# Optimization experiments

Measured on AMD Instinct MI355X. Metric: run time of the kernel, lower is better.

The kernel has to match this reference:

```python
import jax, jax.numpy as jnp
import numpy as np

B = 8192
DIMS = [1024, 1024, 1024, 1024]  # input, hidden0, hidden1, output
RANK = 64


def _apg_layer(x, Wm, bm, U, V, b, activate):
    # hyper-net (MLP_Layer with no hidden units == single Linear): generates rank*rank weights per sample
    w = (x @ Wm.T + bm).reshape(x.shape[0], RANK, RANK)   # [B, r, r]
    u = x @ U.T                                           # U_matrix: [B, r]
    # (u.unsqueeze(-1) * w).sum(-2) == per-sample matvec
    h = jnp.einsum('br,brs->bs', u, w)                    # [B, r]
    out = h @ V.T + b                                     # V_matrix + static bias: [B, out]
    return jax.nn.relu(out) if activate else out


def setup_inputs() -> dict:
    key = jax.random.key(0)
    ks = jax.random.split(key, 16)
    inp = {"x": jax.random.normal(ks[0], (B, DIMS[0]), dtype=jnp.float32)}
    ki = 1
    for l in range(3):
        din, dout = DIMS[l], DIMS[l + 1]
        inp[f"Wm{l}"] = jax.random.normal(ks[ki], (RANK * RANK, din), dtype=jnp.float32) * (1.0 / np.sqrt(din)); ki += 1
        inp[f"bm{l}"] = jnp.zeros((RANK * RANK,), dtype=jnp.float32)
        inp[f"U{l}"] = jax.random.normal(ks[ki], (RANK, din), dtype=jnp.float32) * (1.0 / np.sqrt(din)); ki += 1
        inp[f"V{l}"] = jax.random.normal(ks[ki], (dout, RANK), dtype=jnp.float32) * (1.0 / np.sqrt(RANK)); ki += 1
        inp[f"b{l}"] = jnp.zeros((dout,), dtype=jnp.float32)
    return inp


def reference(x, Wm0, bm0, U0, V0, b0, Wm1, bm1, U1, V1, b1, Wm2, bm2, U2, V2, b2):
    h = _apg_layer(x, Wm0, bm0, U0, V0, b0, activate=True)   # hidden layer 0 + ReLU
    h = _apg_layer(h, Wm1, bm1, U1, V1, b1, activate=True)   # hidden layer 1 + ReLU
    out = _apg_layer(h, Wm2, bm2, U2, V2, b2, activate=False)  # output layer, no activation
    return out
```

## Files before the change

kernel.cpp:

```cpp
#include <hip/hip_runtime.h>
#include <stdint.h>

typedef short bf16x8_t __attribute__((ext_vector_type(8)));
typedef short bf16x4_t __attribute__((ext_vector_type(4)));
typedef float f32x4_t __attribute__((ext_vector_type(4)));
typedef unsigned short u16x4_t __attribute__((ext_vector_type(4)));

#define DEV static __device__ __forceinline__

DEV float bf2f(unsigned short u) {
  union { unsigned int i; float f; } v; v.i = ((unsigned int)u) << 16; return v.f;
}
DEV unsigned short f2bf(float f) {
  union { float f; unsigned int i; } v; v.f = f;
  unsigned int x = v.i;
  unsigned int lsb = (x >> 16) & 1u;
  x += 0x7fffu + lsb;
  return (unsigned short)(x >> 16);
}

__global__ __launch_bounds__(256) void cvt_f32_bf16_k(
    const float* __restrict__ src, unsigned short* __restrict__ dst, int n4) {
  int i = blockIdx.x * 256 + threadIdx.x;
  if (i >= n4) return;
  float4 val = ((const float4*)src)[i];
  u16x4_t o = { f2bf(val.x), f2bf(val.y), f2bf(val.z), f2bf(val.w) };
  *(u16x4_t*)&dst[i * 4] = o;
}

__global__ __launch_bounds__(256) void build_u_k(
    const float* __restrict__ U, unsigned short* __restrict__ dst) {
  int i = blockIdx.x * 256 + threadIdx.x;
  int e = i * 4;
  int row = e >> 10;
  int k = e & 1023;
  float4 v = (row < 64) ? *(const float4*)&U[(size_t)row * 1024 + k]
                        : make_float4(0.f, 0.f, 0.f, 0.f);
  u16x4_t o = { f2bf(v.x), f2bf(v.y), f2bf(v.z), f2bf(v.w) };
  *(u16x4_t*)&dst[e] = o;
}

template <int OUTF32, int RELU, int BIAS>
__global__ __launch_bounds__(256, 2) void gemm_bt(
    const unsigned short* __restrict__ A, const unsigned short* __restrict__ B,
    const float* __restrict__ bias, void* __restrict__ Cout,
    int M, int N, int K) {
  __shared__ unsigned short As[128 * 64];
  __shared__ unsigned short Bs[128 * 64];

  const int tid = threadIdx.x;
  const int lane = tid & 63;
  const int w = tid >> 6;
  const int wrow0 = (w & 1) * 64;
  const int wcol0 = (w >> 1) * 64;
  const int rowBase = blockIdx.y * 128;
  const int colBase = blockIdx.x * 128;

  const int rl = lane >> 3;
  const int kbs = lane & 7;
  const int kbg = kbs ^ rl;

  const int fr = lane & 15;
  const int quad = lane >> 4;

  f32x4_t acc[4][4];
#pragma unroll
  for (int i = 0; i < 4; i++)
#pragma unroll
    for (int j = 0; j < 4; j++) acc[i][j] = f32x4_t{0.f, 0.f, 0.f, 0.f};

  for (int kt = 0; kt < K; kt += 64) {
    __syncthreads();
#pragma unroll
    for (int jj = 0; jj < 4; ++jj) {
      int tr = w * 32 + jj * 8 + rl;
      const unsigned short* ga = A + (size_t)(rowBase + tr) * K + kt + kbg * 8;
      const unsigned short* gb = B + (size_t)(colBase + tr) * K + kt + kbg * 8;
      __builtin_amdgcn_global_load_lds(
          (const __attribute__((address_space(1))) void*)ga,
          (__attribute__((address_space(3))) void*)&As[(w * 32 + jj * 8) * 64],
          16, 0, 0);
      __builtin_amdgcn_global_load_lds(
          (const __attribute__((address_space(1))) void*)gb,
          (__attribute__((address_space(3))) void*)&Bs[(w * 32 + jj * 8) * 64],
          16, 0, 0);
    }
    __syncthreads();

#pragma unroll
    for (int ks = 0; ks < 2; ++ks) {
      bf16x8_t a[4], b[4];
#pragma unroll
      for (int i = 0; i < 4; i++) {
        int m = wrow0 + i * 16 + fr;
        int slot = (ks * 4 + quad) ^ (m & 7);
        a[i] = *(const bf16x8_t*)&As[m * 64 + slot * 8];
      }
#pragma unroll
      for (int j = 0; j < 4; j++) {
        int n = wcol0 + j * 16 + fr;
        int slot = (ks * 4 + quad) ^ (n & 7);
        b[j] = *(const bf16x8_t*)&Bs[n * 64 + slot * 8];
      }
#pragma unroll
      for (int i = 0; i < 4; i++)
#pragma unroll
        for (int j = 0; j < 4; j++)
          acc[i][j] = __builtin_amdgcn_mfma_f32_16x16x32_bf16(a[i], b[j],
                                                              acc[i][j], 0, 0, 0);
    }
  }

#pragma unroll
  for (int j = 0; j < 4; j++) {
    int col = colBase + wcol0 + j * 16 + fr;
    float bv = BIAS ? bias[col] : 0.0f;
#pragma unroll
    for (int i = 0; i < 4; i++) {
#pragma unroll
      for (int r = 0; r < 4; r++) {
        int row = rowBase + wrow0 + i * 16 + quad * 4 + r;
        float v = acc[i][j][r] + bv;
        if (RELU) v = v > 0.f ? v : 0.f;
        if (OUTF32)
          ((float*)Cout)[(size_t)row * N + col] = v;
        else
          ((unsigned short*)Cout)[(size_t)row * N + col] = f2bf(v);
      }
    }
  }
}

__global__ __launch_bounds__(256, 2) void gemm_fused(
    const unsigned short* __restrict__ A,
    const unsigned short* __restrict__ Wmb,
    const unsigned short* __restrict__ ug,
    const float* __restrict__ bm,
    unsigned short* __restrict__ h_out) {
  __shared__ unsigned short smem[16384];
  unsigned short* As = smem;
  unsigned short* Bs = smem + 8192;
  const int K = 1024;

  const int tid = threadIdx.x;
  const int lane = tid & 63;
  const int w = tid >> 6;
  const int wrow0 = (w & 1) * 64;
  const int wcol0 = (w >> 1) * 64;
  const int rowBase = blockIdx.y * 128;
  const int colBase = blockIdx.x * 128;

  const int rl = lane >> 3;
  const int kbs = lane & 7;
  const int kbg = kbs ^ rl;

  const int fr = lane & 15;
  const int quad = lane >> 4;

  f32x4_t acc[4][4];
#pragma unroll
  for (int i = 0; i < 4; i++)
#pragma unroll
    for (int j = 0; j < 4; j++) acc[i][j] = f32x4_t{0.f, 0.f, 0.f, 0.f};

  for (int kt = 0; kt < K; kt += 64) {
    __syncthreads();
#pragma unroll
    for (int jj = 0; jj < 4; ++jj) {
      int tr = w * 32 + jj * 8 + rl;
      int ct = colBase + tr;
      int pr = ((ct & 63) << 6) | (ct >> 6);
      const unsigned short* ga = A + (size_t)(rowBase + tr) * K + kt + kbg * 8;
      const unsigned short* gb = Wmb + (size_t)pr * K + kt + kbg * 8;
      __builtin_amdgcn_global_load_lds(
          (const __attribute__((address_space(1))) void*)ga,
          (__attribute__((address_space(3))) void*)&As[(w * 32 + jj * 8) * 64],
          16, 0, 0);
      __builtin_amdgcn_global_load_lds(
          (const __attribute__((address_space(1))) void*)gb,
          (__attribute__((address_space(3))) void*)&Bs[(w * 32 + jj * 8) * 64],
          16, 0, 0);
    }
    __syncthreads();

#pragma unroll
    for (int ks = 0; ks < 2; ++ks) {
      bf16x8_t a[4], b[4];
#pragma unroll
      for (int i = 0; i < 4; i++) {
        int m = wrow0 + i * 16 + fr;
        int slot = (ks * 4 + quad) ^ (m & 7);
        a[i] = *(const bf16x8_t*)&As[m * 64 + slot * 8];
      }
#pragma unroll
      for (int j = 0; j < 4; j++) {
        int n = wcol0 + j * 16 + fr;
        int slot = (ks * 4 + quad) ^ (n & 7);
        b[j] = *(const bf16x8_t*)&Bs[n * 64 + slot * 8];
      }
#pragma unroll
      for (int i = 0; i < 4; i++)
#pragma unroll
        for (int j = 0; j < 4; j++)
          acc[i][j] = __builtin_amdgcn_mfma_f32_16x16x32_bf16(a[i], b[j],
                                                              acc[i][j], 0, 0, 0);
    }
  }

  __syncthreads();

  {
    int row = tid >> 1;
    int c0 = (tid & 1) * 32;
    const unsigned short* up = ug + (size_t)(rowBase + row) * 128 + c0;
    bf16x8_t v0 = *(const bf16x8_t*)(up);
    bf16x8_t v1 = *(const bf16x8_t*)(up + 8);
    bf16x8_t v2 = *(const bf16x8_t*)(up + 16);
    bf16x8_t v3 = *(const bf16x8_t*)(up + 24);
#pragma unroll
    for (int m = 0; m < 8; m++) {
      smem[(c0 + m) * 136 + row] = (unsigned short)v0[m];
      smem[(c0 + 8 + m) * 136 + row] = (unsigned short)v1[m];
      smem[(c0 + 16 + m) * 136 + row] = (unsigned short)v2[m];
      smem[(c0 + 24 + m) * 136 + row] = (unsigned short)v3[m];
    }
  }
  __syncthreads();

  const int s = blockIdx.x * 2 + (w >> 1);
  float bmv[4];
#pragma unroll
  for (int j = 0; j < 4; j++) bmv[j] = bm[(j * 16 + fr) * 64 + s];

#pragma unroll
  for (int i = 0; i < 4; i++) {
    int row0 = wrow0 + i * 16 + quad * 4;
    bf16x4_t uv[4];
#pragma unroll
    for (int j = 0; j < 4; j++)
      uv[j] = *(const bf16x4_t*)&smem[(j * 16 + fr) * 136 + row0];
#pragma unroll
    for (int r = 0; r < 4; r++) {
      float p = 0.f;
#pragma unroll
      for (int j = 0; j < 4; j++)
        p += bf2f((unsigned short)uv[j][r]) * (acc[i][j][r] + bmv[j]);
      p += __shfl_xor(p, 1, 64);
      p += __shfl_xor(p, 2, 64);
      p += __shfl_xor(p, 4, 64);
      p += __shfl_xor(p, 8, 64);
      if (fr == 0)
        h_out[(size_t)(rowBase + row0 + r) * 64 + s] = f2bf(p);
    }
  }
}

extern "C" void kernel_launch(void* const* d_in, const int* in_sizes, int n_in,
                              void* d_out, int out_size, void* d_ws,
                              size_t ws_size, hipStream_t stream) {
  const float* x = (const float*)d_in[0];
  const float* Wm[3] = {(const float*)d_in[1], (const float*)d_in[6], (const float*)d_in[11]};
  const float* bm[3] = {(const float*)d_in[2], (const float*)d_in[7], (const float*)d_in[12]};
  const float* U[3]  = {(const float*)d_in[3], (const float*)d_in[8], (const float*)d_in[13]};
  const float* V[3]  = {(const float*)d_in[4], (const float*)d_in[9], (const float*)d_in[14]};
  const float* bs[3] = {(const float*)d_in[5], (const float*)d_in[10], (const float*)d_in[15]};

  char* p = (char*)d_ws;
  unsigned short* xb = (unsigned short*)p;  p += 8192UL * 1024 * 2;
  unsigned short* act = (unsigned short*)p; p += 8192UL * 1024 * 2;
  unsigned short* Wmb[3];
  for (int l = 0; l < 3; l++) { Wmb[l] = (unsigned short*)p; p += 4096UL * 1024 * 2; }
  unsigned short* Ub[3];
  for (int l = 0; l < 3; l++) { Ub[l] = (unsigned short*)p; p += 128UL * 1024 * 2; }
  unsigned short* Vb[3];
  for (int l = 0; l < 3; l++) { Vb[l] = (unsigned short*)p; p += 1024UL * 64 * 2; }
  unsigned short* hb = (unsigned short*)p;  p += 8192UL * 64 * 2;
  unsigned short* ug = (unsigned short*)p;  p += 8192UL * 128 * 2;

  cvt_f32_bf16_k<<<8192, 256, 0, stream>>>(x, xb, 8192 * 1024 / 4);
  for (int l = 0; l < 3; l++) {
    cvt_f32_bf16_k<<<4096, 256, 0, stream>>>(Wm[l], Wmb[l], 4096 * 1024 / 4);
    build_u_k<<<128, 256, 0, stream>>>(U[l], Ub[l]);
    cvt_f32_bf16_k<<<64, 256, 0, stream>>>(V[l], Vb[l], 1024 * 64 / 4);
  }

  const unsigned short* cur = xb;
  for (int l = 0; l < 3; l++) {
    gemm_bt<0, 0, 0><<<dim3(1, 64), 256, 0, stream>>>(
        cur, Ub[l], nullptr, ug, 8192, 128, 1024);
    gemm_fused<<<dim3(32, 64), 256, 0, stream>>>(cur, Wmb[l], ug, bm[l], hb);
    if (l < 2) {
      gemm_bt<0, 1, 1><<<dim3(8, 64), 256, 0, stream>>>(
          hb, Vb[l], bs[l], act, 8192, 1024, 64);
      cur = act;
    } else {
      gemm_bt<1, 0, 1><<<dim3(8, 64), 256, 0, stream>>>(
          hb, Vb[2], bs[2], d_out, 8192, 1024, 64);
    }
  }
}
```

Measured before the change: 464.6 us.

## Split-K the u projection, drop U padding, and merge weight conversions into one launch

The u = x·Uᵀ GEMM used to run on only 64 blocks with a 128-wide N that was zero-padded from 64. It now runs as a split-K kernel over 256 blocks, each covering 256 of K with N=64, and a separate reduce kernel sums the four fp32 partials and converts the result to bf16. The ten separate f32-to-bf16 conversion launches are merged into one table-driven kernel. This adds an fp32 partial buffer round trip and one extra launch per layer, in exchange for better CU occupancy and no wasted padded columns.

New measurement: 422.1 us. 9.1% less time.

```diff
diff --git a/kernel.cpp b/kernel.cpp
--- a/kernel.cpp
+++ b/kernel.cpp
@@ -19,25 +19,120 @@
   return (unsigned short)(x >> 16);
 }
 
-__global__ __launch_bounds__(256) void cvt_f32_bf16_k(
-    const float* __restrict__ src, unsigned short* __restrict__ dst, int n4) {
+struct CvtTab {
+  const float* src[10];
+  unsigned short* dst[10];
+  int bstart[10];
+};
+
+__global__ __launch_bounds__(256) void cvt_all_k(CvtTab t) {
+  int bi = blockIdx.x;
+  int seg = 0;
+#pragma unroll
+  for (int s = 1; s < 10; s++) seg += (bi >= t.bstart[s]) ? 1 : 0;
+  int local = (bi - t.bstart[seg]) * 256 + threadIdx.x;
+  const float* src = t.src[seg];
+  unsigned short* dst = t.dst[seg];
+  float4 v = ((const float4*)src)[local];
+  u16x4_t o = { f2bf(v.x), f2bf(v.y), f2bf(v.z), f2bf(v.w) };
+  *(u16x4_t*)&dst[local * 4] = o;
+}
+
+__global__ __launch_bounds__(256, 2) void u_splitk(
+    const unsigned short* __restrict__ A,
+    const unsigned short* __restrict__ Ub,
+    float* __restrict__ part) {
+  __shared__ unsigned short As[128 * 64];
+  __shared__ unsigned short Us[64 * 64];
+
+  const int tid = threadIdx.x;
+  const int lane = tid & 63;
+  const int w = tid >> 6;
+  const int rowBase = blockIdx.y * 128;
+  const int kBase = blockIdx.x * 256;
+
+  const int rl = lane >> 3;
+  const int kbs = lane & 7;
+  const int kbg = kbs ^ rl;
+  const int fr = lane & 15;
+  const int quad = lane >> 4;
+
+  f32x4_t acc[2][4];
+#pragma unroll
+  for (int i = 0; i < 2; i++)
+#pragma unroll
+    for (int j = 0; j < 4; j++) acc[i][j] = f32x4_t{0.f, 0.f, 0.f, 0.f};
+
+  for (int kt = kBase; kt < kBase + 256; kt += 64) {
+    __syncthreads();
+#pragma unroll
+    for (int jj = 0; jj < 4; ++jj) {
+      int tr = w * 32 + jj * 8 + rl;
+      const unsigned short* ga = A + (size_t)(rowBase + tr) * 1024 + kt + kbg * 8;
+      __builtin_amdgcn_global_load_lds(
+          (const __attribute__((address_space(1))) void*)ga,
+          (__attribute__((address_space(3))) void*)&As[(w * 32 + jj * 8) * 64],
+          16, 0, 0);
+    }
+#pragma unroll
+    for (int jj = 0; jj < 2; ++jj) {
+      int tr = w * 16 + jj * 8 + rl;
+      const unsigned short* gu = Ub + (size_t)tr * 1024 + kt + kbg * 8;
+      __builtin_amdgcn_global_load_lds(
+          (const __attribute__((address_space(1))) void*)gu,
+          (__attribute__((address_space(3))) void*)&Us[(w * 16 + jj * 8) * 64],
+          16, 0, 0);
+    }
+    __syncthreads();
+
+#pragma unroll
+    for (int ks = 0; ks < 2; ++ks) {
+      bf16x8_t a[2], b[4];
+#pragma unroll
+      for (int i = 0; i < 2; i++) {
+        int m = w * 32 + i * 16 + fr;
+        int slot = (ks * 4 + quad) ^ (m & 7);
+        a[i] = *(const bf16x8_t*)&As[m * 64 + slot * 8];
+      }
+#pragma unroll
+      for (int j = 0; j < 4; j++) {
+        int n = j * 16 + fr;
+        int slot = (ks * 4 + quad) ^ (n & 7);
+        b[j] = *(const bf16x8_t*)&Us[n * 64 + slot * 8];
+      }
+#pragma unroll
+      for (int i = 0; i < 2; i++)
+#pragma unroll
+        for (int j = 0; j < 4; j++)
+          acc[i][j] = __builtin_amdgcn_mfma_f32_16x16x32_bf16(a[i], b[j],
+                                                              acc[i][j], 0, 0, 0);
+    }
+  }
+
+  float* pp = part + ((size_t)blockIdx.x * 8192 + rowBase) * 64;
+#pragma unroll
+  for (int i = 0; i < 2; i++)
+#pragma unroll
+    for (int j = 0; j < 4; j++)
+#pragma unroll
+      for (int r = 0; r < 4; r++) {
+        int row = w * 32 + i * 16 + quad * 4 + r;
+        pp[(size_t)row * 64 + j * 16 + fr] = acc[i][j][r];
+      }
+}
+
+__global__ __launch_bounds__(256) void u_reduce_k(
+    const float* __restrict__ part, unsigned short* __restrict__ ug) {
   int i = blockIdx.x * 256 + threadIdx.x;
-  if (i >= n4) return;
-  float4 val = ((const float4*)src)[i];
-  u16x4_t o = { f2bf(val.x), f2bf(val.y), f2bf(val.z), f2bf(val.w) };
-  *(u16x4_t*)&dst[i * 4] = o;
-}
-
-__global__ __launch_bounds__(256) void build_u_k(
-    const float* __restrict__ U, unsigned short* __restrict__ dst) {
-  int i = blockIdx.x * 256 + threadIdx.x;
-  int e = i * 4;
-  int row = e >> 10;
-  int k = e & 1023;
-  float4 v = (row < 64) ? *(const float4*)&U[(size_t)row * 1024 + k]
-                        : make_float4(0.f, 0.f, 0.f, 0.f);
-  u16x4_t o = { f2bf(v.x), f2bf(v.y), f2bf(v.z), f2bf(v.w) };
-  *(u16x4_t*)&dst[e] = o;
+  float4 s0 = ((const float4*)part)[i];
+  float4 s1 = ((const float4*)part)[i + 131072];
+  float4 s2 = ((const float4*)part)[i + 262144];
+  float4 s3 = ((const float4*)part)[i + 393216];
+  u16x4_t o = { f2bf(s0.x + s1.x + s2.x + s3.x),
+                f2bf(s0.y + s1.y + s2.y + s3.y),
+                f2bf(s0.z + s1.z + s2.z + s3.z),
+                f2bf(s0.w + s1.w + s2.w + s3.w) };
+  *(u16x4_t*)&ug[i * 4] = o;
 }
 
 template <int OUTF32, int RELU, int BIAS>
@@ -59,7 +154,6 @@
   const int rl = lane >> 3;
   const int kbs = lane & 7;
   const int kbg = kbs ^ rl;
-
   const int fr = lane & 15;
   const int quad = lane >> 4;
 
@@ -153,7 +247,6 @@
   const int rl = lane >> 3;
   const int kbs = lane & 7;
   const int kbg = kbs ^ rl;
-
   const int fr = lane & 15;
   const int quad = lane >> 4;
 
@@ -212,7 +305,7 @@
   {
     int row = tid >> 1;
     int c0 = (tid & 1) * 32;
-    const unsigned short* up = ug + (size_t)(rowBase + row) * 128 + c0;
+    const unsigned short* up = ug + (size_t)(rowBase + row) * 64 + c0;
     bf16x8_t v0 = *(const bf16x8_t*)(up);
     bf16x8_t v1 = *(const bf16x8_t*)(up + 8);
     bf16x8_t v2 = *(const bf16x8_t*)(up + 16);
@@ -271,23 +364,27 @@
   unsigned short* Wmb[3];
   for (int l = 0; l < 3; l++) { Wmb[l] = (unsigned short*)p; p += 4096UL * 1024 * 2; }
   unsigned short* Ub[3];
-  for (int l = 0; l < 3; l++) { Ub[l] = (unsigned short*)p; p += 128UL * 1024 * 2; }
+  for (int l = 0; l < 3; l++) { Ub[l] = (unsigned short*)p; p += 64UL * 1024 * 2; }
   unsigned short* Vb[3];
   for (int l = 0; l < 3; l++) { Vb[l] = (unsigned short*)p; p += 1024UL * 64 * 2; }
   unsigned short* hb = (unsigned short*)p;  p += 8192UL * 64 * 2;
-  unsigned short* ug = (unsigned short*)p;  p += 8192UL * 128 * 2;
-
-  cvt_f32_bf16_k<<<8192, 256, 0, stream>>>(x, xb, 8192 * 1024 / 4);
-  for (int l = 0; l < 3; l++) {
-    cvt_f32_bf16_k<<<4096, 256, 0, stream>>>(Wm[l], Wmb[l], 4096 * 1024 / 4);
-    build_u_k<<<128, 256, 0, stream>>>(U[l], Ub[l]);
-    cvt_f32_bf16_k<<<64, 256, 0, stream>>>(V[l], Vb[l], 1024 * 64 / 4);
-  }
+  unsigned short* ug = (unsigned short*)p;  p += 8192UL * 64 * 2;
+  float* ug_part = (float*)p;               p += 4UL * 8192 * 64 * 4;
+
+  CvtTab t;
+  t.src[0] = x;  t.dst[0] = xb;
+  for (int l = 0; l < 3; l++) { t.src[1 + l] = Wm[l]; t.dst[1 + l] = Wmb[l]; }
+  for (int l = 0; l < 3; l++) { t.src[4 + l] = U[l];  t.dst[4 + l] = Ub[l]; }
+  for (int l = 0; l < 3; l++) { t.src[7 + l] = V[l];  t.dst[7 + l] = Vb[l]; }
+  int bs_tab[10] = {8192, 4096, 4096, 4096, 64, 64, 64, 64, 64, 64};
+  int acc_b = 0;
+  for (int s = 0; s < 10; s++) { t.bstart[s] = acc_b; acc_b += bs_tab[s]; }
+  cvt_all_k<<<acc_b, 256, 0, stream>>>(t);
 
   const unsigned short* cur = xb;
   for (int l = 0; l < 3; l++) {
-    gemm_bt<0, 0, 0><<<dim3(1, 64), 256, 0, stream>>>(
-        cur, Ub[l], nullptr, ug, 8192, 128, 1024);
+    u_splitk<<<dim3(4, 64), 256, 0, stream>>>(cur, Ub[l], ug_part);
+    u_reduce_k<<<512, 256, 0, stream>>>(ug_part, ug);
     gemm_fused<<<dim3(32, 64), 256, 0, stream>>>(cur, Wmb[l], ug, bm[l], hb);
     if (l < 2) {
       gemm_bt<0, 1, 1><<<dim3(8, 64), 256, 0, stream>>>(
```
